# Kernel tuning notes

Hardware: AMD Instinct MI355X
Metric: run time of the kernel (lower is better)

The kernel has to match this reference:

```python
import jax, jax.numpy as jnp
import numpy as np

B, T, H = 8, 4096, 1024
K, V = 128, 128
OUT = 1024

def setup_inputs() -> dict:
    key = jax.random.key(0)
    k1, k2, k3, k4, k5 = jax.random.split(key, 5)
    s = 1.0 / np.sqrt(H)
    return {
        "hidden_state": jax.random.normal(k1, (B, T, H), dtype=jnp.float32),
        "W_proj": jax.random.normal(k2, (H, 3 * K + V), dtype=jnp.float32) * s,
        "b_proj": jax.random.normal(k3, (3 * K + V,), dtype=jnp.float32) * 0.01,
        "W_out": jax.random.normal(k4, (V, OUT), dtype=jnp.float32) * (1.0 / np.sqrt(V)),
        "b_out": jax.random.normal(k5, (OUT,), dtype=jnp.float32) * 0.01,
    }

def reference(hidden_state, W_proj, b_proj, W_out, b_out):
    # fused projection over all timesteps at once: (B,T,3K+V)
    qkgv = jnp.einsum("bth,hd->btd", hidden_state, W_proj) + b_proj
    q, k, g, v = jnp.split(qkgv, [K, 2 * K, 3 * K], axis=-1)
    k = jax.nn.sigmoid(k)
    g = jax.nn.sigmoid(g)

    # time-major for scan: (T,B,*)
    xs = (jnp.swapaxes(q, 0, 1), jnp.swapaxes(k, 0, 1),
          jnp.swapaxes(g, 0, 1), jnp.swapaxes(v, 0, 1))
    cell0 = jnp.zeros((B, K, V), dtype=hidden_state.dtype)

    def step(cell, x):
        q_i, k_i, g_i, v_i = x
        # gated outer-product state update: cell (B,K,V)
        cell = cell * g_i[:, :, None] + k_i[:, :, None] * v_i[:, None, :]
        # query readout: (B,V)
        o_i = jnp.einsum("bkv,bk->bv", cell, q_i)
        return cell, o_i

    final_state, outs = jax.lax.scan(step, cell0, xs)
    outputs = jnp.swapaxes(outs, 0, 1)  # (B,T,V)
    outputs = jnp.einsum("btv,vo->bto", outputs, W_out) + b_out
    return outputs, final_state
```

## Files before the change

### kernel.cpp

```cpp
#include <hip/hip_runtime.h>
#include <math.h>

#define B_ 8
#define T_ 4096
#define H_ 1024
#define K_ 128
#define V_ 128
#define OUT_ 1024
#define NPROJ 512
#define M_ (B_*T_)
#define CC 32
#define NC 128

typedef __attribute__((ext_vector_type(8))) short bf16x8;
typedef __attribute__((ext_vector_type(4))) float f32x4;

__device__ inline unsigned short f2bf(float f){
  union{float f; unsigned int u;} x; x.f = f;
  unsigned int r = x.u + 0x7fff + ((x.u>>16)&1);
  return (unsigned short)(r>>16);
}
__device__ inline float bf2f(unsigned short u){
  union{unsigned int i; float f;} x; x.i = ((unsigned int)u)<<16; return x.f;
}

#define GL16(gp, lp) __builtin_amdgcn_global_load_lds(\
  (const __attribute__((address_space(1))) unsigned int*)(gp), \
  (__attribute__((address_space(3))) unsigned int*)(lp), 16, 0, 0)

#define MFMA16(a,b,c) __builtin_amdgcn_mfma_f32_16x16x32_bf16((a),(b),(c),0,0,0)

__global__ __launch_bounds__(256)
void convT(const float* __restrict__ src, unsigned short* __restrict__ dst,
           int Kd, int N) {
  __shared__ float t[32][33];
  int tx = threadIdx.x & 31, ty = threadIdx.x >> 5;
  int n0 = blockIdx.x * 32, k0 = blockIdx.y * 32;
  #pragma unroll
  for (int r=0;r<4;r++){
    int k = ty*4 + r;
    t[k][tx] = src[(long)(k0+k)*N + n0 + tx];
  }
  __syncthreads();
  #pragma unroll
  for (int r=0;r<4;r++){
    int n = ty*4 + r;
    dst[(long)(n0+n)*Kd + k0 + tx] = f2bf(t[tx][n]);
  }
}

__global__ __launch_bounds__(512, 4)
void proj_mfma4(const float* __restrict__ A, const unsigned short* __restrict__ Bt,
                const float* __restrict__ bias,
                unsigned short* __restrict__ qbf, unsigned short* __restrict__ kbf,
                float* __restrict__ gf, unsigned short* __restrict__ vbf) {
  __shared__ unsigned short sA[128*72];
  __shared__ unsigned short sB[256*64];
  int tid = threadIdx.x, lane = tid & 63, wid = tid >> 6;
  int wm = wid >> 2, wn = wid & 3;
  int l16 = lane & 15, g8 = (lane >> 4) * 8;
  long row0 = (long)blockIdx.y * 128;
  int col0 = blockIdx.x * 256;

  int arow = tid >> 2, acol0 = (tid & 3) * 16;
  const float* Ab = A + (row0 + arow) * 1024 + acol0;
  int srowB = lane >> 3;
  int scolB = (((lane & 7) ^ (srowB & 7)) * 8);

  f32x4 acc[4][4];
  #pragma unroll
  for (int i=0;i<4;i++)
    #pragma unroll
    for (int j=0;j<4;j++) acc[i][j] = (f32x4){0.f,0.f,0.f,0.f};

  float4 ra[4];
  #define LDA(k0_) { _Pragma("unroll") \
    for (int j_=0;j_<4;j_++) ra[j_] = *(const float4*)(Ab + (k0_) + j_*4); }
  #define STA() { \
    unsigned short o_[16]; \
    _Pragma("unroll") \
    for (int j_=0;j_<4;j_++){ \
      o_[j_*4+0]=f2bf(ra[j_].x); o_[j_*4+1]=f2bf(ra[j_].y); \
      o_[j_*4+2]=f2bf(ra[j_].z); o_[j_*4+3]=f2bf(ra[j_].w); \
    } \
    *(uint4*)&sA[arow*72 + acol0]     = ((uint4*)o_)[0]; \
    *(uint4*)&sA[arow*72 + acol0 + 8] = ((uint4*)o_)[1]; \
  }
  #define STB(k0_) { _Pragma("unroll") \
    for (int i_=0;i_<4;i_++){ \
      int r_ = wid*32 + i_*8; \
      GL16(Bt + (long)(col0 + r_ + srowB)*1024 + (k0_) + scolB, &sB[r_*64]); \
    } }

  LDA(0);
  for (int t = 0; t < 16; ++t) {
    STA();
    STB(t*64);
    __syncthreads();
    if (t < 15) { LDA(t*64 + 64); }
    #pragma unroll
    for (int kk2 = 0; kk2 < 2; ++kk2) {
      int kk = kk2 * 32;
      bf16x8 af[4], bf[4];
      #pragma unroll
      for (int mi=0;mi<4;mi++)
        af[mi] = *(const bf16x8*)&sA[(wm*64 + mi*16 + l16)*72 + kk + g8];
      #pragma unroll
      for (int ni=0;ni<4;ni++){
        int brow = wn*64 + ni*16 + l16;
        int slot = ((kk + g8) >> 3) ^ (brow & 7);
        bf[ni] = *(const bf16x8*)&sB[brow*64 + slot*8];
      }
      #pragma unroll
      for (int mi=0;mi<4;mi++)
        #pragma unroll
        for (int ni=0;ni<4;ni++)
          acc[mi][ni] = MFMA16(af[mi], bf[ni], acc[mi][ni]);
    }
    __syncthreads();
  }
  #undef LDA
  #undef STA
  #undef STB

  int seg = blockIdx.x*2 + (wn>>1);
  int cbase = (wn&1)*64;
  #pragma unroll
  for (int mi=0;mi<4;mi++){
    #pragma unroll
    for (int ni=0;ni<4;ni++){
      int c = cbase + ni*16 + l16;
      float bsv = bias[seg*128 + c];
      #pragma unroll
      for (int r=0;r<4;r++){
        long grow = row0 + wm*64 + mi*16 + (lane>>4)*4 + r;
        float v = acc[mi][ni][r] + bsv;
        long off = grow*128 + c;
        if (seg == 0)      qbf[off] = f2bf(v);
        else if (seg == 1) kbf[off] = f2bf(1.f/(1.f+__expf(-v)));
        else if (seg == 2) gf[off]  = 1.f/(1.f+__expf(-v));
        else               vbf[off] = f2bf(v);
      }
    }
  }
}

__global__ __launch_bounds__(128)
void prep(const float* __restrict__ gf, unsigned short* __restrict__ qbf,
          unsigned short* __restrict__ kbf, const unsigned short* __restrict__ vbf,
          unsigned short* __restrict__ khT, unsigned short* __restrict__ vT,
          float* __restrict__ Gc) {
  int k = threadIdx.x;
  int c = blockIdx.x, b = blockIdx.y;
  long base = ((long)b*T_ + (long)c*CC) * 128;
  float G = 1.f;
  float kt[CC];
  unsigned short vv[CC];
  #pragma unroll
  for (int t=0;t<CC;++t){
    long off = base + (long)t*128 + k;
    float g = gf[off];
    G *= g;
    float q = bf2f(qbf[off]);
    qbf[off] = f2bf(q*G);
    float kk = bf2f(kbf[off]);
    float ktl = kk/G;
    kbf[off] = f2bf(ktl);
    kt[t] = ktl;
    vv[t] = vbf[off];
  }
  long cb = (long)b*NC + c;
  Gc[cb*128 + k] = G;
  unsigned short ob[CC];
  #pragma unroll
  for (int s=0;s<CC;++s) ob[s] = f2bf(kt[s]*G);
  long tbase = (cb*128 + k)*CC;
  #pragma unroll
  for (int j=0;j<4;j++) *(uint4*)(khT + tbase + j*8) = *(uint4*)(ob + j*8);
  #pragma unroll
  for (int j=0;j<4;j++) *(uint4*)(vT + tbase + j*8) = *(uint4*)(vv + j*8);
}

__global__ __launch_bounds__(256)
void chunkstate(const unsigned short* __restrict__ khT, const unsigned short* __restrict__ vT,
                unsigned short* __restrict__ Ut) {
  __shared__ unsigned short kS[128][36];
  __shared__ unsigned short vS[128][36];
  int tid = threadIdx.x, lane = tid&63, w = tid>>6;
  long cb = (long)blockIdx.y*NC + blockIdx.x;
  const unsigned short* kg = khT + cb*4096;
  const unsigned short* vg = vT  + cb*4096;
  #pragma unroll
  for (int j=0;j<2;j++){
    int idx = tid + j*256;
    int r = idx>>2, s8 = (idx&3)*8;
    *(uint4*)&kS[r][s8] = *(const uint4*)(kg + r*32 + s8);
    *(uint4*)&vS[r][s8] = *(const uint4*)(vg + r*32 + s8);
  }
  __syncthreads();
  int l16 = lane&15, g8 = (lane>>4)*8;
  bf16x8 af[2], bfr[8];
  #pragma unroll
  for (int i=0;i<2;i++) af[i] = *(const bf16x8*)&vS[w*32 + i*16 + l16][g8];
  #pragma unroll
  for (int j=0;j<8;j++) bfr[j] = *(const bf16x8*)&kS[j*16 + l16][g8];
  #pragma unroll
  for (int i=0;i<2;i++){
    #pragma unroll
    for (int j=0;j<8;j++){
      f32x4 acc = (f32x4){0.f,0.f,0.f,0.f};
      acc = MFMA16(af[i], bfr[j], acc);
      int kcol = j*16 + l16;
      #pragma unroll
      for (int r=0;r<4;r++){
        int vrow = w*32 + i*16 + (lane>>4)*4 + r;
        Ut[cb*16384 + vrow*128 + kcol] = f2bf(acc[r]);
      }
    }
  }
}

__global__ __launch_bounds__(256)
void seqstate(const float* __restrict__ Gc, unsigned short* __restrict__ Ut,
              float* __restrict__ fstate) {
  int idx = blockIdx.x*256 + threadIdx.x;
  int b = blockIdx.y;
  int v = idx>>5, k0 = (idx&31)*4;
  float cell[4] = {0.f,0.f,0.f,0.f};
  long ub = (long)b*NC*16384 + (long)v*128 + k0;
  long gb = (long)b*NC*128 + k0;
  #pragma unroll 2
  for (int c=0; c<NC; ++c){
    uint2 u = *(const uint2*)(Ut + ub + (long)c*16384);
    float4 gc = *(const float4*)(Gc + gb + (long)c*128);
    unsigned short cb4[4] = {f2bf(cell[0]), f2bf(cell[1]), f2bf(cell[2]), f2bf(cell[3])};
    *(uint2*)(Ut + ub + (long)c*16384) = *(uint2*)cb4;
    cell[0] = fmaf(cell[0], gc.x, bf2f((unsigned short)(u.x & 0xffff)));
    cell[1] = fmaf(cell[1], gc.y, bf2f((unsigned short)(u.x >> 16)));
    cell[2] = fmaf(cell[2], gc.z, bf2f((unsigned short)(u.y & 0xffff)));
    cell[3] = fmaf(cell[3], gc.w, bf2f((unsigned short)(u.y >> 16)));
  }
  #pragma unroll
  for (int j=0;j<4;j++)
    fstate[((long)b*128 + k0 + j)*128 + v] = cell[j];
}

#define CP 140
__global__ __launch_bounds__(256)
void chunkout(const unsigned short* __restrict__ qbf, const unsigned short* __restrict__ kbf,
              const unsigned short* __restrict__ vT, const unsigned short* __restrict__ cellT,
              unsigned short* __restrict__ obf) {
  __shared__ unsigned short qS[32][CP];
  __shared__ unsigned short kS[32][CP];
  __shared__ unsigned short cS[128][CP];
  __shared__ unsigned short vS[128][36];
  __shared__ unsigned short pS[4][32][36];
  int tid = threadIdx.x, lane = tid&63, w = tid>>6;
  long cb = (long)blockIdx.y*NC + blockIdx.x;
  const unsigned short* qg = qbf + cb*4096;
  const unsigned short* kg = kbf + cb*4096;
  const unsigned short* vg = vT  + cb*4096;
  const unsigned short* cg = cellT + cb*16384;
  #pragma unroll
  for (int j=0;j<2;j++){
    int idx = tid + j*256;
    int r = idx>>4, c8 = (idx&15)*8;
    *(uint4*)&qS[r][c8] = *(const uint4*)(qg + r*128 + c8);
    *(uint4*)&kS[r][c8] = *(const uint4*)(kg + r*128 + c8);
    int rv = idx>>2, s8 = (idx&3)*8;
    *(uint4*)&vS[rv][s8] = *(const uint4*)(vg + rv*32 + s8);
  }
  #pragma unroll
  for (int j=0;j<8;j++){
    int idx = tid + j*256;
    int r = idx>>4, c8 = (idx&15)*8;
    *(uint4*)&cS[r][c8] = *(const uint4*)(cg + r*128 + c8);
  }
  __syncthreads();

  int l16 = lane&15, g = lane>>4, g8 = g*8;
  f32x4 s00 = (f32x4){0.f,0.f,0.f,0.f}, s01 = s00, s11 = s00;
  #pragma unroll
  for (int ks=0; ks<4; ++ks){
    bf16x8 ka = *(const bf16x8*)&kS[l16][ks*32+g8];
    bf16x8 kb = *(const bf16x8*)&kS[16+l16][ks*32+g8];
    bf16x8 qa = *(const bf16x8*)&qS[l16][ks*32+g8];
    bf16x8 qb = *(const bf16x8*)&qS[16+l16][ks*32+g8];
    s00 = MFMA16(ka, qa, s00);
    s01 = MFMA16(ka, qb, s01);
    s11 = MFMA16(kb, qb, s11);
  }
  pS[w][l16][16 + 4*g + (0)] = 0; pS[w][l16][16 + 4*g + 1] = 0;
  pS[w][l16][16 + 4*g + 2] = 0;   pS[w][l16][16 + 4*g + 3] = 0;
  #pragma unroll
  for (int r=0;r<4;r++){
    int sl = 4*g + r;
    pS[w][l16][sl]       = (l16 >= sl) ? f2bf(s00[r]) : (unsigned short)0;
    pS[w][16+l16][sl]    = f2bf(s01[r]);
    pS[w][16+l16][16+sl] = (l16 >= sl) ? f2bf(s11[r]) : (unsigned short)0;
  }
  f32x4 o[2][2];
  #pragma unroll
  for (int i=0;i<2;i++)
    #pragma unroll
    for (int j=0;j<2;j++) o[i][j] = (f32x4){0.f,0.f,0.f,0.f};
  {
    bf16x8 p0 = *(const bf16x8*)&pS[w][l16][g8];
    bf16x8 p1 = *(const bf16x8*)&pS[w][16+l16][g8];
    bf16x8 v0 = *(const bf16x8*)&vS[w*32 + l16][g8];
    bf16x8 v1 = *(const bf16x8*)&vS[w*32 + 16 + l16][g8];
    o[0][0] = MFMA16(p0, v0, o[0][0]);
    o[0][1] = MFMA16(p0, v1, o[0][1]);
    o[1][0] = MFMA16(p1, v0, o[1][0]);
    o[1][1] = MFMA16(p1, v1, o[1][1]);
  }
  #pragma unroll
  for (int ks=0; ks<4; ++ks){
    bf16x8 qa = *(const bf16x8*)&qS[l16][ks*32+g8];
    bf16x8 qb = *(const bf16x8*)&qS[16+l16][ks*32+g8];
    bf16x8 c0 = *(const bf16x8*)&cS[w*32 + l16][ks*32+g8];
    bf16x8 c1 = *(const bf16x8*)&cS[w*32 + 16 + l16][ks*32+g8];
    o[0][0] = MFMA16(qa, c0, o[0][0]);
    o[0][1] = MFMA16(qa, c1, o[0][1]);
    o[1][0] = MFMA16(qb, c0, o[1][0]);
    o[1][1] = MFMA16(qb, c1, o[1][1]);
  }
  #pragma unroll
  for (int ti=0;ti<2;ti++)
    #pragma unroll
    for (int vi=0;vi<2;vi++)
      #pragma unroll
      for (int r=0;r<4;r++){
        int t = ti*16 + 4*g + r;
        int v = w*32 + vi*16 + l16;
        obf[cb*4096 + (long)t*128 + v] = f2bf(o[ti][vi][r]);
      }
}

__global__ __launch_bounds__(256)
void out_mfma(const unsigned short* __restrict__ A, const unsigned short* __restrict__ Bt,
              const float* __restrict__ bias, float* __restrict__ C) {
  __shared__ unsigned short As[128*32];
  __shared__ unsigned short Bs[128*32];
  int tid = threadIdx.x, lane = tid & 63, wid = tid >> 6;
  long row0 = (long)blockIdx.y * 128;
  int col0 = blockIdx.x * 128;
  f32x4 acc[4][4];
  #pragma unroll
  for (int i=0;i<4;i++)
    #pragma unroll
    for (int j=0;j<4;j++) acc[i][j] = (f32x4){0.f,0.f,0.f,0.f};

  const unsigned short* Ab = A + row0*128;
  const unsigned short* Bb = Bt + (long)col0*128;
  int srow = lane >> 2;
  int soff = (lane & 3) * 8;
  int wrow = (wid>>1)*64, wcol = (wid&1)*64;

  for (int k0 = 0; k0 < 128; k0 += 32) {
    #pragma unroll
    for (int i=0;i<2;i++){
      int r = wid*32 + i*16;
      GL16(Ab + (long)(r + srow)*128 + k0 + soff, &As[r*32]);
      GL16(Bb + (long)(r + srow)*128 + k0 + soff, &Bs[r*32]);
    }
    __syncthreads();
    bf16x8 af[4], bfr[4];
    #pragma unroll
    for (int mi=0;mi<4;mi++)
      af[mi] = *(const bf16x8*)&As[(wrow + mi*16 + (lane&15))*32 + (lane>>4)*8];
    #pragma unroll
    for (int ni=0;ni<4;ni++)
      bfr[ni] = *(const bf16x8*)&Bs[(wcol + ni*16 + (lane&15))*32 + (lane>>4)*8];
    #pragma unroll
    for (int mi=0;mi<4;mi++)
      #pragma unroll
      for (int ni=0;ni<4;ni++)
        acc[mi][ni] = MFMA16(af[mi], bfr[ni], acc[mi][ni]);
    __syncthreads();
  }

  #pragma unroll
  for (int mi=0;mi<4;mi++){
    #pragma unroll
    for (int ni=0;ni<4;ni++){
      int col = col0 + wcol + ni*16 + (lane&15);
      float bsv = bias[col];
      #pragma unroll
      for (int r=0;r<4;r++){
        long grow = row0 + wrow + mi*16 + (lane>>4)*4 + r;
        C[grow*OUT_ + col] = acc[mi][ni][r] + bsv;
      }
    }
  }
}

extern "C" void kernel_launch(void* const* d_in, const int* in_sizes, int n_in,
                              void* d_out, int out_size, void* d_ws, size_t ws_size,
                              hipStream_t stream) {
  const float* hidden = (const float*)d_in[0];
  const float* Wp     = (const float*)d_in[1];
  const float* bp     = (const float*)d_in[2];
  const float* Wo     = (const float*)d_in[3];
  const float* bo     = (const float*)d_in[4];
  float* out    = (float*)d_out;
  float* fstate = out + (long)M_ * OUT_;

  char* w = (char*)d_ws;
  unsigned short* khT   = (unsigned short*)w;
  unsigned short* vT    = (unsigned short*)(w + 8388608);
  float*          Gc    = (float*)(w + 16777216);
  unsigned short* Ut    = (unsigned short*)(w + 17301504);
  unsigned short* obf   = (unsigned short*)(w + 50855936);
  unsigned short* Wot = (unsigned short*)(w + 67108864);
  unsigned short* Wpt = (unsigned short*)(w + 67371008);
  unsigned short* qbf = (unsigned short*)(w + 68419584);
  unsigned short* kbf = (unsigned short*)(w + 76808192);
  unsigned short* vbf = (unsigned short*)(w + 85196800);
  float*          gf  = (float*)(w + 93585408);

  convT<<<dim3(NPROJ/32, H_/32), 256, 0, stream>>>(Wp, Wpt, H_, NPROJ);
  convT<<<dim3(OUT_/32, V_/32), 256, 0, stream>>>(Wo, Wot, V_, OUT_);
  proj_mfma4<<<dim3(2, 256), 512, 0, stream>>>(hidden, Wpt, bp, qbf, kbf, gf, vbf);
  prep<<<dim3(NC, B_), 128, 0, stream>>>(gf, qbf, kbf, vbf, khT, vT, Gc);
  chunkstate<<<dim3(NC, B_), 256, 0, stream>>>(khT, vT, Ut);
  seqstate<<<dim3(16, B_), 256, 0, stream>>>(Gc, Ut, fstate);
  chunkout<<<dim3(NC, B_), 256, 0, stream>>>(qbf, kbf, vT, Ut, obf);
  out_mfma<<<dim3(8, 256), 256, 0, stream>>>(obf, Wot, bo, out);
}
```

Measured before the change: 182.8 us.

## Double-buffer LDS in projection GEMM with explicit waitcnt/barrier software pipeline

Rewrites the projection GEMM main loop to use two LDS buffers for A and B. Global loads for future k-tiles, their bf16 conversion and stores now overlap the MFMAs on the current tile, using two register staging sets, manual s_waitcnt/s_barrier with sched_barrier fences, and s_setprio around the MFMA block. The aim is to hide global-load and barrier latency in the compute-bound proj stage. In exchange it doubles LDS use (launch bounds drop from 4 to 2 blocks per CU) and holds more fragment registers, which may reduce occupancy.

```diff
diff --git a/kernel.cpp b/kernel.cpp
--- a/kernel.cpp
+++ b/kernel.cpp
@@ -49,13 +49,13 @@
   }
 }
 
-__global__ __launch_bounds__(512, 4)
-void proj_mfma4(const float* __restrict__ A, const unsigned short* __restrict__ Bt,
+__global__ __launch_bounds__(512, 2)
+void proj_mfma5(const float* __restrict__ A, const unsigned short* __restrict__ Bt,
                 const float* __restrict__ bias,
                 unsigned short* __restrict__ qbf, unsigned short* __restrict__ kbf,
                 float* __restrict__ gf, unsigned short* __restrict__ vbf) {
-  __shared__ unsigned short sA[128*72];
-  __shared__ unsigned short sB[256*64];
+  __shared__ unsigned short sA[2][128*72];
+  __shared__ unsigned short sB[2][256*64];
   int tid = threadIdx.x, lane = tid & 63, wid = tid >> 6;
   int wm = wid >> 2, wn = wid & 3;
   int l16 = lane & 15, g8 = (lane >> 4) * 8;
@@ -65,7 +65,7 @@
   int arow = tid >> 2, acol0 = (tid & 3) * 16;
   const float* Ab = A + (row0 + arow) * 1024 + acol0;
   int srowB = lane >> 3;
-  int scolB = (((lane & 7) ^ (srowB & 7)) * 8);
+  int scolB = ((lane & 7) ^ srowB) * 8;
 
   f32x4 acc[4][4];
   #pragma unroll
@@ -73,55 +73,85 @@
     #pragma unroll
     for (int j=0;j<4;j++) acc[i][j] = (f32x4){0.f,0.f,0.f,0.f};
 
-  float4 ra[4];
-  #define LDA(k0_) { _Pragma("unroll") \
-    for (int j_=0;j_<4;j_++) ra[j_] = *(const float4*)(Ab + (k0_) + j_*4); }
-  #define STA() { \
+  float4 raA[4], raB[4];
+  bf16x8 af[2][4], bf[2][4];
+
+  #define LDA(dst_, k0_) { _Pragma("unroll") \
+    for (int j_=0;j_<4;j_++) dst_[j_] = *(const float4*)(Ab + (k0_) + j_*4); }
+  #define STA(bi_, src_) { \
     unsigned short o_[16]; \
     _Pragma("unroll") \
     for (int j_=0;j_<4;j_++){ \
-      o_[j_*4+0]=f2bf(ra[j_].x); o_[j_*4+1]=f2bf(ra[j_].y); \
-      o_[j_*4+2]=f2bf(ra[j_].z); o_[j_*4+3]=f2bf(ra[j_].w); \
+      o_[j_*4+0]=f2bf(src_[j_].x); o_[j_*4+1]=f2bf(src_[j_].y); \
+      o_[j_*4+2]=f2bf(src_[j_].z); o_[j_*4+3]=f2bf(src_[j_].w); \
     } \
-    *(uint4*)&sA[arow*72 + acol0]     = ((uint4*)o_)[0]; \
-    *(uint4*)&sA[arow*72 + acol0 + 8] = ((uint4*)o_)[1]; \
-  }
-  #define STB(k0_) { _Pragma("unroll") \
+    *(uint4*)&sA[bi_][arow*72 + acol0]     = ((uint4*)o_)[0]; \
+    *(uint4*)&sA[bi_][arow*72 + acol0 + 8] = ((uint4*)o_)[1]; \
+  }
+  #define STB(bi_, k0_) { _Pragma("unroll") \
     for (int i_=0;i_<4;i_++){ \
       int r_ = wid*32 + i_*8; \
-      GL16(Bt + (long)(col0 + r_ + srowB)*1024 + (k0_) + scolB, &sB[r_*64]); \
+      GL16(Bt + (long)(col0 + r_ + srowB)*1024 + (k0_) + scolB, &sB[bi_][r_*64]); \
     } }
-
-  LDA(0);
-  for (int t = 0; t < 16; ++t) {
-    STA();
-    STB(t*64);
-    __syncthreads();
-    if (t < 15) { LDA(t*64 + 64); }
-    #pragma unroll
-    for (int kk2 = 0; kk2 < 2; ++kk2) {
-      int kk = kk2 * 32;
-      bf16x8 af[4], bf[4];
-      #pragma unroll
-      for (int mi=0;mi<4;mi++)
-        af[mi] = *(const bf16x8*)&sA[(wm*64 + mi*16 + l16)*72 + kk + g8];
-      #pragma unroll
-      for (int ni=0;ni<4;ni++){
-        int brow = wn*64 + ni*16 + l16;
-        int slot = ((kk + g8) >> 3) ^ (brow & 7);
-        bf[ni] = *(const bf16x8*)&sB[brow*64 + slot*8];
-      }
-      #pragma unroll
-      for (int mi=0;mi<4;mi++)
-        #pragma unroll
-        for (int ni=0;ni<4;ni++)
-          acc[mi][ni] = MFMA16(af[mi], bf[ni], acc[mi][ni]);
-    }
-    __syncthreads();
-  }
+  #define FRAGS(bi_) { _Pragma("unroll") \
+    for (int kk2_=0;kk2_<2;kk2_++){ int kk_ = kk2_*32; \
+      _Pragma("unroll") \
+      for (int mi_=0;mi_<4;mi_++) \
+        af[kk2_][mi_] = *(const bf16x8*)&sA[bi_][(wm*64 + mi_*16 + l16)*72 + kk_ + g8]; \
+      _Pragma("unroll") \
+      for (int ni_=0;ni_<4;ni_++){ \
+        int brow_ = wn*64 + ni_*16 + l16; \
+        int slot_ = ((kk_ + g8) >> 3) ^ (brow_ & 7); \
+        bf[kk2_][ni_] = *(const bf16x8*)&sB[bi_][brow_*64 + slot_*8]; \
+      } \
+    } }
+  #define MFMAS { __builtin_amdgcn_s_setprio(1); \
+    _Pragma("unroll") \
+    for (int kk2_=0;kk2_<2;kk2_++) \
+      _Pragma("unroll") \
+      for (int mi_=0;mi_<4;mi_++) \
+        _Pragma("unroll") \
+        for (int ni_=0;ni_<4;ni_++) \
+          acc[mi_][ni_] = MFMA16(af[kk2_][mi_], bf[kk2_][ni_], acc[mi_][ni_]); \
+    __builtin_amdgcn_s_setprio(0); }
+  #define BARA() { asm volatile("s_waitcnt lgkmcnt(0)" ::: "memory"); \
+    __builtin_amdgcn_sched_barrier(0); __builtin_amdgcn_s_barrier(); \
+    __builtin_amdgcn_sched_barrier(0); }
+  #define BARB(n_) { asm volatile("s_waitcnt vmcnt(" #n_ ") lgkmcnt(0)" ::: "memory"); \
+    __builtin_amdgcn_sched_barrier(0); __builtin_amdgcn_s_barrier(); \
+    __builtin_amdgcn_sched_barrier(0); }
+
+  LDA(raA, 0);
+  LDA(raB, 64);
+  STB(0, 0);
+  STA(0, raA);
+  LDA(raA, 128);
+  STB(1, 64);
+  asm volatile("s_waitcnt vmcnt(8) lgkmcnt(0)" ::: "memory");
+  __builtin_amdgcn_sched_barrier(0);
+  __builtin_amdgcn_s_barrier();
+  __builtin_amdgcn_sched_barrier(0);
+
+  for (int t2 = 0; t2 < 12; t2 += 2) {
+    FRAGS(0); BARA();
+    STA(1, raB); LDA(raB, (t2+3)*64); STB(0, (t2+2)*64);
+    MFMAS; BARB(8);
+    FRAGS(1); BARA();
+    STA(0, raA); LDA(raA, (t2+4)*64); STB(1, (t2+3)*64);
+    MFMAS; BARB(8);
+  }
+  FRAGS(0); BARA(); STA(1, raB); LDA(raB, 15*64); STB(0, 14*64); MFMAS; BARB(8);
+  FRAGS(1); BARA(); STA(0, raA); STB(1, 15*64); MFMAS; BARB(4);
+  FRAGS(0); BARA(); STA(1, raB); MFMAS; BARB(0);
+  FRAGS(1); MFMAS;
+
   #undef LDA
   #undef STA
   #undef STB
+  #undef FRAGS
+  #undef MFMAS
+  #undef BARA
+  #undef BARB
 
   int seg = blockIdx.x*2 + (wn>>1);
   int cbase = (wn&1)*64;
@@ -421,7 +451,7 @@
 
   convT<<<dim3(NPROJ/32, H_/32), 256, 0, stream>>>(Wp, Wpt, H_, NPROJ);
   convT<<<dim3(OUT_/32, V_/32), 256, 0, stream>>>(Wo, Wot, V_, OUT_);
-  proj_mfma4<<<dim3(2, 256), 512, 0, stream>>>(hidden, Wpt, bp, qbf, kbf, gf, vbf);
+  proj_mfma5<<<dim3(2, 256), 512, 0, stream>>>(hidden, Wpt, bp, qbf, kbf, gf, vbf);
   prep<<<dim3(NC, B_), 128, 0, stream>>>(gf, qbf, kbf, vbf, khT, vT, Gc);
   chunkstate<<<dim3(NC, B_), 256, 0, stream>>>(khT, vT, Ut);
   seqstate<<<dim3(16, B_), 256, 0, stream>>>(Gc, Ut, fstate);
```

Measured after the change: 207.5 us. 13.5% more time.

## Split sequential chunk-state scan into segmented two-pass parallel scan

Applied to the files above, without the earlier changes.

The inter-chunk state recurrence, which used to run serially over all 128 chunks in 128 blocks, is now split into 8 segments. A first kernel computes each segment's local state and cumulative gate product. A second kernel combines the prefixes of earlier segments and then replays its own segment to write chunk-start states. This raises parallelism from 128 to 1024 blocks and shortens the dependent chain, at the cost of reading Ut twice, an extra launch, and writing segment buffers to workspace.

```diff
diff --git a/kernel.cpp b/kernel.cpp
--- a/kernel.cpp
+++ b/kernel.cpp
@@ -221,16 +221,53 @@
 }
 
 __global__ __launch_bounds__(256)
-void seqstate(const float* __restrict__ Gc, unsigned short* __restrict__ Ut,
-              float* __restrict__ fstate) {
+void seqstate_a(const float* __restrict__ Gc, const unsigned short* __restrict__ Ut,
+                float* __restrict__ segB, float* __restrict__ segG) {
   int idx = blockIdx.x*256 + threadIdx.x;
-  int b = blockIdx.y;
+  int s = blockIdx.y, b = blockIdx.z;
   int v = idx>>5, k0 = (idx&31)*4;
   float cell[4] = {0.f,0.f,0.f,0.f};
+  float gp[4] = {1.f,1.f,1.f,1.f};
   long ub = (long)b*NC*16384 + (long)v*128 + k0;
   long gb = (long)b*NC*128 + k0;
-  #pragma unroll 2
-  for (int c=0; c<NC; ++c){
+  int c0 = s*16;
+  #pragma unroll 4
+  for (int c=c0; c<c0+16; ++c){
+    uint2 u = *(const uint2*)(Ut + ub + (long)c*16384);
+    float4 gc = *(const float4*)(Gc + gb + (long)c*128);
+    cell[0] = fmaf(cell[0], gc.x, bf2f((unsigned short)(u.x & 0xffff)));
+    cell[1] = fmaf(cell[1], gc.y, bf2f((unsigned short)(u.x >> 16)));
+    cell[2] = fmaf(cell[2], gc.z, bf2f((unsigned short)(u.y & 0xffff)));
+    cell[3] = fmaf(cell[3], gc.w, bf2f((unsigned short)(u.y >> 16)));
+    gp[0] *= gc.x; gp[1] *= gc.y; gp[2] *= gc.z; gp[3] *= gc.w;
+  }
+  long sb = ((long)b*8 + s)*16384 + (long)v*128 + k0;
+  *(float4*)(segB + sb) = make_float4(cell[0],cell[1],cell[2],cell[3]);
+  if (v == 0)
+    *(float4*)(segG + ((long)b*8 + s)*128 + k0) = make_float4(gp[0],gp[1],gp[2],gp[3]);
+}
+
+__global__ __launch_bounds__(256)
+void seqstate_b(const float* __restrict__ Gc, unsigned short* __restrict__ Ut,
+                const float* __restrict__ segB, const float* __restrict__ segG,
+                float* __restrict__ fstate) {
+  int idx = blockIdx.x*256 + threadIdx.x;
+  int s = blockIdx.y, b = blockIdx.z;
+  int v = idx>>5, k0 = (idx&31)*4;
+  float cell[4] = {0.f,0.f,0.f,0.f};
+  for (int sp=0; sp<s; ++sp){
+    float4 bg = *(const float4*)(segG + ((long)b*8 + sp)*128 + k0);
+    float4 bb = *(const float4*)(segB + ((long)b*8 + sp)*16384 + (long)v*128 + k0);
+    cell[0] = fmaf(cell[0], bg.x, bb.x);
+    cell[1] = fmaf(cell[1], bg.y, bb.y);
+    cell[2] = fmaf(cell[2], bg.z, bb.z);
+    cell[3] = fmaf(cell[3], bg.w, bb.w);
+  }
+  long ub = (long)b*NC*16384 + (long)v*128 + k0;
+  long gb = (long)b*NC*128 + k0;
+  int c0 = s*16;
+  #pragma unroll 4
+  for (int c=c0; c<c0+16; ++c){
     uint2 u = *(const uint2*)(Ut + ub + (long)c*16384);
     float4 gc = *(const float4*)(Gc + gb + (long)c*128);
     unsigned short cb4[4] = {f2bf(cell[0]), f2bf(cell[1]), f2bf(cell[2]), f2bf(cell[3])};
@@ -240,9 +277,11 @@
     cell[2] = fmaf(cell[2], gc.z, bf2f((unsigned short)(u.y & 0xffff)));
     cell[3] = fmaf(cell[3], gc.w, bf2f((unsigned short)(u.y >> 16)));
   }
-  #pragma unroll
-  for (int j=0;j<4;j++)
-    fstate[((long)b*128 + k0 + j)*128 + v] = cell[j];
+  if (s == 7){
+    #pragma unroll
+    for (int j=0;j<4;j++)
+      fstate[((long)b*128 + k0 + j)*128 + v] = cell[j];
+  }
 }
 
 #define CP 140
@@ -412,6 +451,8 @@
   float*          Gc    = (float*)(w + 16777216);
   unsigned short* Ut    = (unsigned short*)(w + 17301504);
   unsigned short* obf   = (unsigned short*)(w + 50855936);
+  float*          segB  = (float*)(w + 59244544);
+  float*          segG  = (float*)(w + 63438848);
   unsigned short* Wot = (unsigned short*)(w + 67108864);
   unsigned short* Wpt = (unsigned short*)(w + 67371008);
   unsigned short* qbf = (unsigned short*)(w + 68419584);
@@ -424,7 +465,8 @@
   proj_mfma4<<<dim3(2, 256), 512, 0, stream>>>(hidden, Wpt, bp, qbf, kbf, gf, vbf);
   prep<<<dim3(NC, B_), 128, 0, stream>>>(gf, qbf, kbf, vbf, khT, vT, Gc);
   chunkstate<<<dim3(NC, B_), 256, 0, stream>>>(khT, vT, Ut);
-  seqstate<<<dim3(16, B_), 256, 0, stream>>>(Gc, Ut, fstate);
+  seqstate_a<<<dim3(16, 8, B_), 256, 0, stream>>>(Gc, Ut, segB, segG);
+  seqstate_b<<<dim3(16, 8, B_), 256, 0, stream>>>(Gc, Ut, segB, segG, fstate);
   chunkout<<<dim3(NC, B_), 256, 0, stream>>>(qbf, kbf, vT, Ut, obf);
   out_mfma<<<dim3(8, 256), 256, 0, stream>>>(obf, Wot, bo, out);
 }
```

Result: no change. 180.2 us (-1.4%).
